# Performance work log

Hardware: AMD Instinct MI355X
Metric: run time of the kernel (lower is better)

The kernel has to match this reference:

```python
import jax, jax.numpy as jnp
import numpy as np

C = 64
K = 3          # kernel_size
EK = 5         # encoder_kernel
PAD = (K - 1) // 2


def _conv(x, w, pad):
    return jax.lax.conv_general_dilated(
        x, w, window_strides=(1, 1), padding=[(pad, pad), (pad, pad)],
        dimension_numbers=('NCHW', 'OIHW', 'NCHW'))


def setup_inputs() -> dict:
    key = jax.random.key(0)
    ks = jax.random.split(key, 6)
    b, h, w = 8, 128, 128
    x = jax.random.normal(ks[0], (b, C, h, w), dtype=jnp.float32)
    # gen_kernel: 1x1 conv (C->C, with bias) then EKxEK conv (C->K*K, no bias)
    w1 = jax.random.normal(ks[1], (C, C, 1, 1), dtype=jnp.float32) * (1.0 / np.sqrt(C))
    b1 = jax.random.normal(ks[2], (C,), dtype=jnp.float32) * 0.01
    w2 = jax.random.normal(ks[3], (K * K, C, EK, EK), dtype=jnp.float32) * (1.0 / np.sqrt(C * EK * EK))
    # consensus t_c: 1x1 conv C->C//4, relu, 1x1 conv C//4->C, relu (no bias)
    tc1 = jax.random.normal(ks[4], (C // 4, C, 1, 1), dtype=jnp.float32) * (1.0 / np.sqrt(C))
    tc2 = jax.random.normal(ks[5], (C, C // 4, 1, 1), dtype=jnp.float32) * (1.0 / np.sqrt(C // 4))
    return {"x": x, "w1": w1, "b1": b1, "w2": w2, "tc1": tc1, "tc2": tc2}


def reference(x, w1, b1, w2, tc1, tc2):
    b, c, h, w = x.shape
    oh, ow = h, w  # stride == 1
    # dynamic kernel logits: (b, K*K, oh, ow)
    y = _conv(x, w1, 0) + b1[None, :, None, None]
    wt = _conv(y, w2, (EK - 1) // 2)
    # consensus scale: adaptive avg pool to 1x1 then mean over batch -> (c,)
    x_con = jnp.mean(x, axis=(0, 2, 3))                      # (c,)
    h1 = jax.nn.relu(jnp.einsum('oc,c->o', tc1[:, :, 0, 0], x_con))
    tmp = jax.nn.relu(jnp.einsum('oc,c->o', tc2[:, :, 0, 0], h1))  # (c,)
    # broadcast logits to (b, c, K*K, oh, ow) and softmax over K*K
    logits = wt[:, None, :, :, :] * tmp[None, :, None, None, None]
    attn = jax.nn.softmax(logits, axis=2)                    # (b,c,9,oh,ow)
    # unfold patches: reflect-pad then 9 shifted views, order kh*K+kw (row-major)
    px = jnp.pad(x, ((0, 0), (0, 0), (PAD, PAD), (PAD, PAD)), mode='reflect')
    pats = jnp.stack([px[:, :, i:i + oh, j:j + ow]
                      for i in range(K) for j in range(K)], axis=2)  # (b,c,9,oh,ow)
    out = jnp.sum(attn * pats, axis=2)                       # (b,c,oh,ow)
    return out
```

## Files before the change

### kernel.cpp

```cpp
#include <hip/hip_runtime.h>
#include <hip/hip_bf16.h>
#include <cstddef>


#define B 8
#define C 64
#define HW 128
#define NK 9
#define NT 25
#define XR 132
#define TI 8
#define TJ 16
#define HR 12
#define HC 20

typedef __attribute__((ext_vector_type(8))) short short8;
typedef __attribute__((ext_vector_type(4))) float float4v;
typedef __attribute__((ext_vector_type(2))) float float2v;
typedef __attribute__((ext_vector_type(4))) unsigned int uint4v;

__device__ __forceinline__ unsigned short f2bf(float f) {
    unsigned int u = __float_as_uint(f);
    unsigned int r = u + 0x7FFF + ((u >> 16) & 1);
    return (unsigned short)(r >> 16);
}
__device__ __forceinline__ float fast_rcp(float x) {
    float r;
    asm("v_rcp_f32 %0, %1" : "=v"(r) : "v"(x));
    return r;
}
__device__ __forceinline__ void load_lds16(const unsigned short* g, unsigned short* l) {
    __builtin_amdgcn_global_load_lds(
        (const __attribute__((address_space(1))) unsigned int*)g,
        (__attribute__((address_space(3))) unsigned int*)l,
        16, 0, 0);
}

__global__ __launch_bounds__(256) void xpack_kernel(const float* __restrict__ x,
                                                    const float* __restrict__ w1,
                                                    const float* __restrict__ b1,
                                                    const float* __restrict__ w2,
                                                    unsigned short* __restrict__ xbf,
                                                    float* __restrict__ part_rows,
                                                    unsigned short* __restrict__ Abuf,
                                                    float* __restrict__ betaG) {
    __shared__ float sw2[NK * 64];
    __shared__ float sw1[64 * 32];
    __shared__ float beta_s[NT * NK];
    const int t = threadIdx.x;
    if (blockIdx.x >= XR) {
        const int id = (blockIdx.x - XR) * B + blockIdx.y;
        if (id < 50) {
            const int chunk = id;
            const int tt = chunk >> 1, ch = chunk & 1;
            for (int idx = t; idx < NK * 64; idx += 256) {
                const int m = idx >> 6, cc = idx & 63;
                sw2[idx] = w2[(m * 64 + cc) * NT + tt];
            }
            for (int idx = t; idx < 2048; idx += 256) {
                const int cc = idx >> 5, j = idx & 31;
                sw1[idx] = w1[cc * 64 + ch * 32 + j];
            }
            __syncthreads();
            for (int sidx = 0; sidx < 2; ++sidx) {
                const int slot = sidx * 256 + t;
                const int quad = slot >> 7, m = (slot >> 3) & 15, jj = slot & 7;
                unsigned short hi = 0;
                if (m < NK) {
                    float s = 0.f;
                    for (int cc = 0; cc < 64; ++cc)
                        s += sw2[m * 64 + cc] * sw1[cc * 32 + quad * 8 + jj];
                    hi = f2bf(s);
                }
                Abuf[chunk * 512 + slot] = hi;
            }
        } else if (id == 50) {
            if (t < NT * NK) {
                const int tt = t / NK, k = t - tt * NK;
                float s = 0.f;
                for (int cc = 0; cc < 64; ++cc)
                    s += w2[(k * 64 + cc) * NT + tt] * b1[cc];
                beta_s[t] = s;
            }
            __syncthreads();
            if (t < 225) {
                const int ic = t / 45, jc = (t / 9) % 5, k = t % 9;
                float s = 0.f;
                for (int eh = 0; eh < 5; ++eh) {
                    bool rok = (ic == 0) ? (eh >= 2) : (ic == 1) ? (eh >= 1)
                              : (ic == 3) ? (eh <= 3) : (ic == 4) ? (eh <= 2) : true;
                    if (!rok) continue;
                    for (int ew = 0; ew < 5; ++ew) {
                        bool cok = (jc == 0) ? (ew >= 2) : (jc == 1) ? (ew >= 1)
                                  : (jc == 3) ? (ew <= 3) : (jc == 4) ? (ew <= 2) : true;
                        if (cok) s += beta_s[(eh * 5 + ew) * NK + k];
                    }
                }
                betaG[t] = s;
            }
        }
        return;
    }
    const int r = blockIdx.x, b = blockIdx.y;
    unsigned short* rowp = xbf + ((size_t)(b * XR + r)) * (XR * 64);
    if (r < 2 || r >= 130) {
        const uint4v z = {0u, 0u, 0u, 0u};
        for (int idx = t; idx < 1056; idx += 256)
            *(uint4v*)(rowp + idx * 8) = z;
        return;
    }
    const int h = r - 2;
    if (t < 32) {
        const uint4v z = {0u, 0u, 0u, 0u};
        const int q4 = t & 3;
        const int wc = (q4 < 2) ? q4 : (q4 + 128);
        *(uint4v*)(rowp + wc * 64 + ((t >> 2) << 3)) = z;
    }
    const int c8 = t >> 5;
    const int wl = t & 31;
    const float* xp = x + (((size_t)(b * C + c8 * 8)) * HW + h) * HW;
    float s8[8] = {0.f, 0.f, 0.f, 0.f, 0.f, 0.f, 0.f, 0.f};
#pragma unroll
    for (int k = 0; k < 4; ++k) {
        const int gw = wl + 32 * k;
        const int wc = gw + 2;
        uint4v dv;
#pragma unroll
        for (int j = 0; j < 4; ++j) {
            const float v0 = xp[(size_t)(2 * j) * (HW * HW) + gw];
            const float v1 = xp[(size_t)(2 * j + 1) * (HW * HW) + gw];
            s8[2 * j] += v0;
            s8[2 * j + 1] += v1;
            dv[j] = (unsigned int)f2bf(v0) | ((unsigned int)f2bf(v1) << 16);
        }
        const int sw = ((r & 1) * 4 + wc) & 7;
        *(uint4v*)(rowp + wc * 64 + ((c8 ^ sw) << 3)) = dv;
    }
#pragma unroll
    for (int off = 16; off > 0; off >>= 1) {
#pragma unroll
        for (int j = 0; j < 8; ++j) s8[j] += __shfl_down(s8[j], off);
    }
    if (wl == 0) {
        float* pr = part_rows + ((size_t)(b * HW + h)) * 64 + c8 * 8;
#pragma unroll
        for (int j = 0; j < 8; ++j) pr[j] = s8[j];
    }
}

__global__ __launch_bounds__(256) void prep2_kernel(const float* __restrict__ part_rows,
                                                    const float* __restrict__ tc1,
                                                    const float* __restrict__ tc2,
                                                    float* __restrict__ ltg) {
    __shared__ float pl[256];
    const int c = threadIdx.x >> 2, seg = threadIdx.x & 3;
    const float* pr = part_rows + (size_t)(seg * 256) * 64 + c;
    float s0 = 0.f, s1 = 0.f, s2 = 0.f, s3 = 0.f;
#pragma unroll 4
    for (int i = 0; i < 256; i += 4) {
        s0 += pr[(size_t)(i + 0) * 64];
        s1 += pr[(size_t)(i + 1) * 64];
        s2 += pr[(size_t)(i + 2) * 64];
        s3 += pr[(size_t)(i + 3) * 64];
    }
    pl[threadIdx.x] = (s0 + s1) + (s2 + s3);
    __syncthreads();
    if (threadIdx.x < 64) {
        const int lane = threadIdx.x;
        float xcv = (pl[lane * 4 + 0] + pl[lane * 4 + 1]
                   + pl[lane * 4 + 2] + pl[lane * 4 + 3]) * (1.f / (B * HW * HW));
        float hh = 0.f;
        for (int c2 = 0; c2 < C; ++c2) {
            float xcc = __shfl(xcv, c2);
            if (lane < 16) hh += tc1[lane * C + c2] * xcc;
        }
        hh = fmaxf(hh, 0.f);
        float ltv = 0.f;
#pragma unroll
        for (int o = 0; o < 16; ++o) {
            float ho = __shfl(hh, o);
            ltv += tc2[lane * 16 + o] * ho;
        }
        ltg[lane] = fmaxf(ltv, 0.f);
    }
}

__global__ __launch_bounds__(256, 4) void fused_kernel(const unsigned short* __restrict__ xbf,
                                                       const unsigned short* __restrict__ Abuf,
                                                       const float* __restrict__ betaG,
                                                       const float* __restrict__ ltg,
                                                       float* __restrict__ out) {
    __shared__ __align__(16) unsigned short stag[HR * HC * 64];
    __shared__ float wpA[NK * 128];
    __shared__ float wpB[NK * 128];
    const int b = blockIdx.y;
    const int i0 = (blockIdx.x >> 3) * TI, j0 = (blockIdx.x & 7) * TJ;
    const int tid = threadIdx.x, lane = tid & 63, wid = tid >> 6;
    const int n = lane & 15, q = lane >> 4;
    const int rowg = wid >> 1, h = wid & 1;

    {
        const unsigned short* xrow0 = xbf + (((size_t)(b * XR + i0)) * XR + j0) * 64;
#pragma unroll
        for (int k = 0; k < 7; ++k) {
            const int ci = k * 256 + tid;
            const int li = ((ci >> 5) * 205) >> 10;
            const int rem = ci - li * 160;
            load_lds16(xrow0 + li * (XR * 64) + rem * 8, stag + ci * 8);
        }
        if (tid < 128) {
            const int ci = 1792 + tid;
            const int li = ((ci >> 5) * 205) >> 10;
            const int rem = ci - li * 160;
            load_lds16(xrow0 + li * (XR * 64) + rem * 8, stag + ci * 8);
        }
    }

    const int prow = rowg * 4 + q;
    const int pgi = i0 + prow, pgj = j0 + n;
    float bgv[NK];
    if (h == 0) {
        const int ic = pgi < 2 ? pgi : (pgi > 125 ? pgi - 123 : 2);
        const int jc = pgj < 2 ? pgj : (pgj > 125 ? pgj - 123 : 2);
        const float* bp = betaG + (ic * 5 + jc) * NK;
#pragma unroll
        for (int k = 0; k < NK; ++k) bgv[k] = bp[k];
    }

    __syncthreads();

    float4v acc[4];
    const float4v zero4 = {0.f, 0.f, 0.f, 0.f};
#pragma unroll
    for (int g = 0; g < 4; ++g) acc[g] = zero4;

    const unsigned short* Ab = Abuf + h * 512 + lane * 8;
    const int chs = (h << 2) | q;
    const int rb = rowg * 4;
#pragma unroll
    for (int ew = 0; ew < 5; ++ew) {
        short8 w8[8];
#pragma unroll
        for (int rr = 0; rr < 8; ++rr) {
            const int px = (rb + rr) * HC + ew + n;
            w8[rr] = *(const short8*)(stag + px * 64 + ((chs ^ (px & 7)) << 3));
        }
#pragma unroll
        for (int eh = 0; eh < 5; ++eh) {
            const int t = eh * 5 + ew;
            const short8 ahi = *(const short8*)(Ab + t * 1024);
#pragma unroll
            for (int g = 0; g < 4; ++g)
                acc[g] = __builtin_amdgcn_mfma_f32_16x16x32_bf16(ahi, w8[g + eh], acc[g], 0, 0, 0);
        }
    }

    float wv[NK];
#pragma unroll
    for (int k = 0; k < NK; ++k) {
        const int src = (k >> 2) * 16 + n;
        const int rr = k & 3;
        float v0 = __shfl(acc[0][rr], src);
        float v1 = __shfl(acc[1][rr], src);
        float v2 = __shfl(acc[2][rr], src);
        float v3 = __shfl(acc[3][rr], src);
        wv[k] = (q == 0) ? v0 : (q == 1) ? v1 : (q == 2) ? v2 : v3;
    }

    const int slot = rowg * 64 + lane;
    if (h == 0) {
#pragma unroll
        for (int k = 0; k < NK; ++k) wpA[k * 128 + slot] = wv[k] + bgv[k];
    } else {
#pragma unroll
        for (int k = 0; k < NK; ++k) wpB[k * 128 + slot] = wv[k];
    }
    __syncthreads();

#pragma unroll
    for (int sp = 0; sp < 2; ++sp) {
        const int lpx = lane + (sp << 6);
        const int brow = lpx >> 4, bcol = lpx & 15;
        const int bgi = i0 + brow, bgj = j0 + bcol;
        float2v dvp[NK], dv2p[NK];
        float ps1 = 0.f, ps2 = 0.f;
#pragma unroll
        for (int k = 0; k < NK; ++k) {
            const float d = wpA[k * 128 + lpx] + wpB[k * 128 + lpx];
            const float d2 = d * d;
            ps1 += d; ps2 += d2;
            dvp[k][0] = d;  dvp[k][1] = d;
            dv2p[k][0] = d2; dv2p[k][1] = d2;
        }
        float2v ps1p; ps1p[0] = ps1; ps1p[1] = ps1;
        float2v ps2p; ps2p[0] = ps2; ps2p[1] = ps2;
        const float2v ninep = {9.0f, 9.0f};
        int r0 = bgi - 1; r0 = r0 < 0 ? 1 : r0;
        int r2 = bgi + 1; r2 = r2 > 127 ? 126 : r2;
        int c0 = bgj - 1; c0 = c0 < 0 ? 1 : c0;
        int c2 = bgj + 1; c2 = c2 > 127 ? 126 : c2;
        const int R[3] = {r0 - i0 + 2, bgi - i0 + 2, r2 - i0 + 2};
        const int Cc[3] = {c0 - j0 + 2, bgj - j0 + 2, c2 - j0 + 2};
#pragma unroll
        for (int oc = 0; oc < 2; ++oc) {
            const int oct = wid * 2 + oc;
            uint4v xs[NK];
#pragma unroll
            for (int kh = 0; kh < 3; ++kh)
#pragma unroll
                for (int kw = 0; kw < 3; ++kw) {
                    const int prc = R[kh] * HC + Cc[kw];
                    xs[kh * 3 + kw] = *(const uint4v*)(stag + prc * 64 + ((oct ^ (prc & 7)) << 3));
                }
            float* outp = out + (((size_t)b * C + oct * 8) * HW + bgi) * HW + bgj;
#pragma unroll
            for (int jj = 0; jj < 4; ++jj) {
                const float2v tp = *(const float2v*)(ltg + oct * 8 + jj * 2);
                const float2v tph = tp * 0.5f;
                float2v a0 = {0.f, 0.f}, a1 = {0.f, 0.f}, a2 = {0.f, 0.f};
#pragma unroll
                for (int k = 0; k < NK; ++k) {
                    const unsigned int u = xs[k][jj];
                    float2v xv;
                    xv[0] = __uint_as_float(u << 16);
                    xv[1] = __uint_as_float(u & 0xffff0000u);
                    a0 += xv;
                    a1 = __builtin_elementwise_fma(dvp[k], xv, a1);
                    a2 = __builtin_elementwise_fma(dv2p[k], xv, a2);
                }
                const float2v nump = __builtin_elementwise_fma(
                    tp, __builtin_elementwise_fma(tph, a2, a1), a0);
                const float2v denp = __builtin_elementwise_fma(
                    tp, __builtin_elementwise_fma(tph, ps2p, ps1p), ninep);
                outp[(size_t)(jj * 2) * (HW * HW)] = nump[0] * fast_rcp(denp[0]);
                outp[(size_t)(jj * 2 + 1) * (HW * HW)] = nump[1] * fast_rcp(denp[1]);
            }
        }
    }
}

extern "C" void kernel_launch(void* const* d_in, const int* in_sizes, int n_in,
                              void* d_out, int out_size, void* d_ws, size_t ws_size,
                              hipStream_t stream) {
    const float* x   = (const float*)d_in[0];
    const float* w1  = (const float*)d_in[1];
    const float* b1  = (const float*)d_in[2];
    const float* w2  = (const float*)d_in[3];
    const float* tc1 = (const float*)d_in[4];
    const float* tc2 = (const float*)d_in[5];
    float* out = (float*)d_out;

    char* ws = (char*)d_ws;
    float* ltg   = (float*)(ws + 0);
    unsigned short* Abuf = (unsigned short*)(ws + 1024);
    float* betaG = (float*)(ws + 53248);
    float* part_rows = (float*)(ws + 54272);
    unsigned short* xbf  = (unsigned short*)(ws + 316416);

    xpack_kernel<<<dim3(XR + 7, B), 256, 0, stream>>>(x, w1, b1, w2, xbf, part_rows, Abuf, betaG);
    prep2_kernel<<<1, 256, 0, stream>>>(part_rows, tc1, tc2, ltg);
    fused_kernel<<<dim3(128, B), 256, 0, stream>>>(xbf, Abuf, betaG, ltg, out);
}
```

Baseline: 127.2 us.

## Process two row tiles per block, sharing halo rows and prefetching second tile

Each block now covers 16 output rows as two sequential 8-row sub-tiles instead of one 8-row tile, halving the grid. The second sub-tile reuses four halo rows already staged in LDS and loads only eight new rows into a second buffer, issued after the first sync so the load overlaps the first sub-tile's compute. This cuts redundant halo loads and per-block setup. The cost is higher LDS use, launch bounds lowered to 2 blocks per CU, fewer blocks overall, and an extra barrier between sub-tiles.

```diff
diff --git a/kernel.cpp b/kernel.cpp
--- a/kernel.cpp
+++ b/kernel.cpp
@@ -185,16 +185,18 @@
     }
 }
 
-__global__ __launch_bounds__(256, 4) void fused_kernel(const unsigned short* __restrict__ xbf,
+__global__ __launch_bounds__(256, 2) void fused_kernel(const unsigned short* __restrict__ xbf,
                                                        const unsigned short* __restrict__ Abuf,
                                                        const float* __restrict__ betaG,
                                                        const float* __restrict__ ltg,
                                                        float* __restrict__ out) {
-    __shared__ __align__(16) unsigned short stag[HR * HC * 64];
+    __shared__ __align__(16) unsigned short stag0[HR * HC * 64];
+    __shared__ __align__(16) unsigned short stag1[8 * HC * 64];
     __shared__ float wpA[NK * 128];
     __shared__ float wpB[NK * 128];
     const int b = blockIdx.y;
-    const int i0 = (blockIdx.x >> 3) * TI, j0 = (blockIdx.x & 7) * TJ;
+    const int bx = blockIdx.x;
+    const int i0 = (bx >> 3) * 16, j0 = (bx & 7) * TJ;
     const int tid = threadIdx.x, lane = tid & 63, wid = tid >> 6;
     const int n = lane & 15, q = lane >> 4;
     const int rowg = wid >> 1, h = wid & 1;
@@ -206,134 +208,162 @@
             const int ci = k * 256 + tid;
             const int li = ((ci >> 5) * 205) >> 10;
             const int rem = ci - li * 160;
-            load_lds16(xrow0 + li * (XR * 64) + rem * 8, stag + ci * 8);
+            load_lds16(xrow0 + li * (XR * 64) + rem * 8, stag0 + ci * 8);
         }
         if (tid < 128) {
             const int ci = 1792 + tid;
             const int li = ((ci >> 5) * 205) >> 10;
             const int rem = ci - li * 160;
-            load_lds16(xrow0 + li * (XR * 64) + rem * 8, stag + ci * 8);
-        }
-    }
-
-    const int prow = rowg * 4 + q;
-    const int pgi = i0 + prow, pgj = j0 + n;
-    float bgv[NK];
-    if (h == 0) {
-        const int ic = pgi < 2 ? pgi : (pgi > 125 ? pgi - 123 : 2);
-        const int jc = pgj < 2 ? pgj : (pgj > 125 ? pgj - 123 : 2);
-        const float* bp = betaG + (ic * 5 + jc) * NK;
-#pragma unroll
-        for (int k = 0; k < NK; ++k) bgv[k] = bp[k];
-    }
-
+            load_lds16(xrow0 + li * (XR * 64) + rem * 8, stag0 + ci * 8);
+        }
+    }
     __syncthreads();
 
-    float4v acc[4];
-    const float4v zero4 = {0.f, 0.f, 0.f, 0.f};
-#pragma unroll
-    for (int g = 0; g < 4; ++g) acc[g] = zero4;
+    {
+        const unsigned short* xrow1 = xbf + (((size_t)(b * XR + i0 + 12)) * XR + j0) * 64;
+#pragma unroll
+        for (int k = 0; k < 5; ++k) {
+            const int ci = k * 256 + tid;
+            const int li = ((ci >> 5) * 205) >> 10;
+            const int rem = ci - li * 160;
+            load_lds16(xrow1 + li * (XR * 64) + rem * 8, stag1 + ci * 8);
+        }
+    }
 
     const unsigned short* Ab = Abuf + h * 512 + lane * 8;
     const int chs = (h << 2) | q;
     const int rb = rowg * 4;
-#pragma unroll
-    for (int ew = 0; ew < 5; ++ew) {
-        short8 w8[8];
-#pragma unroll
-        for (int rr = 0; rr < 8; ++rr) {
-            const int px = (rb + rr) * HC + ew + n;
-            w8[rr] = *(const short8*)(stag + px * 64 + ((chs ^ (px & 7)) << 3));
-        }
-#pragma unroll
-        for (int eh = 0; eh < 5; ++eh) {
-            const int t = eh * 5 + ew;
-            const short8 ahi = *(const short8*)(Ab + t * 1024);
-#pragma unroll
-            for (int g = 0; g < 4; ++g)
-                acc[g] = __builtin_amdgcn_mfma_f32_16x16x32_bf16(ahi, w8[g + eh], acc[g], 0, 0, 0);
-        }
-    }
-
-    float wv[NK];
-#pragma unroll
-    for (int k = 0; k < NK; ++k) {
-        const int src = (k >> 2) * 16 + n;
-        const int rr = k & 3;
-        float v0 = __shfl(acc[0][rr], src);
-        float v1 = __shfl(acc[1][rr], src);
-        float v2 = __shfl(acc[2][rr], src);
-        float v3 = __shfl(acc[3][rr], src);
-        wv[k] = (q == 0) ? v0 : (q == 1) ? v1 : (q == 2) ? v2 : v3;
-    }
-
-    const int slot = rowg * 64 + lane;
-    if (h == 0) {
-#pragma unroll
-        for (int k = 0; k < NK; ++k) wpA[k * 128 + slot] = wv[k] + bgv[k];
-    } else {
-#pragma unroll
-        for (int k = 0; k < NK; ++k) wpB[k * 128 + slot] = wv[k];
-    }
-    __syncthreads();
-
-#pragma unroll
-    for (int sp = 0; sp < 2; ++sp) {
-        const int lpx = lane + (sp << 6);
-        const int brow = lpx >> 4, bcol = lpx & 15;
-        const int bgi = i0 + brow, bgj = j0 + bcol;
-        float2v dvp[NK], dv2p[NK];
-        float ps1 = 0.f, ps2 = 0.f;
+
+#pragma unroll
+    for (int tt = 0; tt < 2; ++tt) {
+        if (tt == 1) __syncthreads();
+        const int i0t = i0 + tt * 8;
+
+        const int prow = rb + q;
+        const int pgi = i0t + prow, pgj = j0 + n;
+        float bgv[NK];
+        if (h == 0) {
+            const int ic = pgi < 2 ? pgi : (pgi > 125 ? pgi - 123 : 2);
+            const int jc = pgj < 2 ? pgj : (pgj > 125 ? pgj - 123 : 2);
+            const float* bp = betaG + (ic * 5 + jc) * NK;
+#pragma unroll
+            for (int k = 0; k < NK; ++k) bgv[k] = bp[k];
+        }
+
+        float4v acc[4];
+        const float4v zero4 = {0.f, 0.f, 0.f, 0.f};
+#pragma unroll
+        for (int g = 0; g < 4; ++g) acc[g] = zero4;
+#pragma unroll
+        for (int ew = 0; ew < 5; ++ew) {
+            short8 w8[8];
+#pragma unroll
+            for (int rr = 0; rr < 8; ++rr) {
+                const int hrow = rb + rr;
+                const unsigned short* sb2;
+                int lr;
+                if (tt == 0) { sb2 = stag0; lr = hrow; }
+                else if (hrow < 4) { sb2 = stag0; lr = hrow + 8; }
+                else { sb2 = stag1; lr = hrow - 4; }
+                const int px = lr * HC + ew + n;
+                w8[rr] = *(const short8*)(sb2 + px * 64 + ((chs ^ (px & 7)) << 3));
+            }
+#pragma unroll
+            for (int eh = 0; eh < 5; ++eh) {
+                const int t = eh * 5 + ew;
+                const short8 ahi = *(const short8*)(Ab + t * 1024);
+#pragma unroll
+                for (int g = 0; g < 4; ++g)
+                    acc[g] = __builtin_amdgcn_mfma_f32_16x16x32_bf16(ahi, w8[g + eh], acc[g], 0, 0, 0);
+            }
+        }
+
+        float wv[NK];
 #pragma unroll
         for (int k = 0; k < NK; ++k) {
-            const float d = wpA[k * 128 + lpx] + wpB[k * 128 + lpx];
-            const float d2 = d * d;
-            ps1 += d; ps2 += d2;
-            dvp[k][0] = d;  dvp[k][1] = d;
-            dv2p[k][0] = d2; dv2p[k][1] = d2;
-        }
-        float2v ps1p; ps1p[0] = ps1; ps1p[1] = ps1;
-        float2v ps2p; ps2p[0] = ps2; ps2p[1] = ps2;
-        const float2v ninep = {9.0f, 9.0f};
-        int r0 = bgi - 1; r0 = r0 < 0 ? 1 : r0;
-        int r2 = bgi + 1; r2 = r2 > 127 ? 126 : r2;
-        int c0 = bgj - 1; c0 = c0 < 0 ? 1 : c0;
-        int c2 = bgj + 1; c2 = c2 > 127 ? 126 : c2;
-        const int R[3] = {r0 - i0 + 2, bgi - i0 + 2, r2 - i0 + 2};
-        const int Cc[3] = {c0 - j0 + 2, bgj - j0 + 2, c2 - j0 + 2};
-#pragma unroll
-        for (int oc = 0; oc < 2; ++oc) {
-            const int oct = wid * 2 + oc;
-            uint4v xs[NK];
-#pragma unroll
-            for (int kh = 0; kh < 3; ++kh)
-#pragma unroll
-                for (int kw = 0; kw < 3; ++kw) {
-                    const int prc = R[kh] * HC + Cc[kw];
-                    xs[kh * 3 + kw] = *(const uint4v*)(stag + prc * 64 + ((oct ^ (prc & 7)) << 3));
+            const int src = (k >> 2) * 16 + n;
+            const int rr = k & 3;
+            float v0 = __shfl(acc[0][rr], src);
+            float v1 = __shfl(acc[1][rr], src);
+            float v2 = __shfl(acc[2][rr], src);
+            float v3 = __shfl(acc[3][rr], src);
+            wv[k] = (q == 0) ? v0 : (q == 1) ? v1 : (q == 2) ? v2 : v3;
+        }
+
+        const int slot = rowg * 64 + lane;
+        if (h == 0) {
+#pragma unroll
+            for (int k = 0; k < NK; ++k) wpA[k * 128 + slot] = wv[k] + bgv[k];
+        } else {
+#pragma unroll
+            for (int k = 0; k < NK; ++k) wpB[k * 128 + slot] = wv[k];
+        }
+        __syncthreads();
+
+#pragma unroll
+        for (int sp = 0; sp < 2; ++sp) {
+            const int lpx = lane + (sp << 6);
+            const int brow = lpx >> 4, bcol = lpx & 15;
+            const int bgi = i0t + brow, bgj = j0 + bcol;
+            float2v dvp[NK], dv2p[NK];
+            float ps1 = 0.f, ps2 = 0.f;
+#pragma unroll
+            for (int k = 0; k < NK; ++k) {
+                const float d = wpA[k * 128 + lpx] + wpB[k * 128 + lpx];
+                const float d2 = d * d;
+                ps1 += d; ps2 += d2;
+                dvp[k][0] = d;  dvp[k][1] = d;
+                dv2p[k][0] = d2; dv2p[k][1] = d2;
+            }
+            float2v ps1p; ps1p[0] = ps1; ps1p[1] = ps1;
+            float2v ps2p; ps2p[0] = ps2; ps2p[1] = ps2;
+            const float2v ninep = {9.0f, 9.0f};
+            int r0 = bgi - 1; r0 = r0 < 0 ? 1 : r0;
+            int r2 = bgi + 1; r2 = r2 > 127 ? 126 : r2;
+            int c0 = bgj - 1; c0 = c0 < 0 ? 1 : c0;
+            int c2 = bgj + 1; c2 = c2 > 127 ? 126 : c2;
+            const int R[3] = {r0 - i0t + 2, bgi - i0t + 2, r2 - i0t + 2};
+            const int Cc[3] = {c0 - j0 + 2, bgj - j0 + 2, c2 - j0 + 2};
+#pragma unroll
+            for (int oc = 0; oc < 2; ++oc) {
+                const int oct = wid * 2 + oc;
+                uint4v xs[NK];
+#pragma unroll
+                for (int kh = 0; kh < 3; ++kh)
+#pragma unroll
+                    for (int kw = 0; kw < 3; ++kw) {
+                        const int hrk = R[kh];
+                        const unsigned short* sb2;
+                        int lr;
+                        if (tt == 0) { sb2 = stag0; lr = hrk; }
+                        else if (hrk < 4) { sb2 = stag0; lr = hrk + 8; }
+                        else { sb2 = stag1; lr = hrk - 4; }
+                        const int prc = lr * HC + Cc[kw];
+                        xs[kh * 3 + kw] = *(const uint4v*)(sb2 + prc * 64 + ((oct ^ (prc & 7)) << 3));
+                    }
+                float* outp = out + (((size_t)b * C + oct * 8) * HW + bgi) * HW + bgj;
+#pragma unroll
+                for (int jj = 0; jj < 4; ++jj) {
+                    const float2v tp = *(const float2v*)(ltg + oct * 8 + jj * 2);
+                    const float2v tph = tp * 0.5f;
+                    float2v a0 = {0.f, 0.f}, a1 = {0.f, 0.f}, a2 = {0.f, 0.f};
+#pragma unroll
+                    for (int k = 0; k < NK; ++k) {
+                        const unsigned int u = xs[k][jj];
+                        float2v xv;
+                        xv[0] = __uint_as_float(u << 16);
+                        xv[1] = __uint_as_float(u & 0xffff0000u);
+                        a0 += xv;
+                        a1 = __builtin_elementwise_fma(dvp[k], xv, a1);
+                        a2 = __builtin_elementwise_fma(dv2p[k], xv, a2);
+                    }
+                    const float2v nump = __builtin_elementwise_fma(
+                        tp, __builtin_elementwise_fma(tph, a2, a1), a0);
+                    const float2v denp = __builtin_elementwise_fma(
+                        tp, __builtin_elementwise_fma(tph, ps2p, ps1p), ninep);
+                    outp[(size_t)(jj * 2) * (HW * HW)] = nump[0] * fast_rcp(denp[0]);
+                    outp[(size_t)(jj * 2 + 1) * (HW * HW)] = nump[1] * fast_rcp(denp[1]);
                 }
-            float* outp = out + (((size_t)b * C + oct * 8) * HW + bgi) * HW + bgj;
-#pragma unroll
-            for (int jj = 0; jj < 4; ++jj) {
-                const float2v tp = *(const float2v*)(ltg + oct * 8 + jj * 2);
-                const float2v tph = tp * 0.5f;
-                float2v a0 = {0.f, 0.f}, a1 = {0.f, 0.f}, a2 = {0.f, 0.f};
-#pragma unroll
-                for (int k = 0; k < NK; ++k) {
-                    const unsigned int u = xs[k][jj];
-                    float2v xv;
-                    xv[0] = __uint_as_float(u << 16);
-                    xv[1] = __uint_as_float(u & 0xffff0000u);
-                    a0 += xv;
-                    a1 = __builtin_elementwise_fma(dvp[k], xv, a1);
-                    a2 = __builtin_elementwise_fma(dv2p[k], xv, a2);
-                }
-                const float2v nump = __builtin_elementwise_fma(
-                    tp, __builtin_elementwise_fma(tph, a2, a1), a0);
-                const float2v denp = __builtin_elementwise_fma(
-                    tp, __builtin_elementwise_fma(tph, ps2p, ps1p), ninep);
-                outp[(size_t)(jj * 2) * (HW * HW)] = nump[0] * fast_rcp(denp[0]);
-                outp[(size_t)(jj * 2 + 1) * (HW * HW)] = nump[1] * fast_rcp(denp[1]);
             }
         }
     }
@@ -359,5 +389,5 @@
 
     xpack_kernel<<<dim3(XR + 7, B), 256, 0, stream>>>(x, w1, b1, w2, xbf, part_rows, Abuf, betaG);
     prep2_kernel<<<1, 256, 0, stream>>>(part_rows, tc1, tc2, ltg);
-    fused_kernel<<<dim3(128, B), 256, 0, stream>>>(xbf, Abuf, betaG, ltg, out);
-}
+    fused_kernel<<<dim3(64, B), 256, 0, stream>>>(xbf, Abuf, betaG, ltg, out);
+}
```

Measured after the change: 129.5 us. Within noise of the previous version (+1.8%).
